# Optimization experiments

Measured on AMD Instinct MI355X. Metric: run time of the kernel, lower is better.

Reference implementation:

```python
import jax, jax.numpy as jnp
import numpy as np

B, N, M = 32, 512, 32          # batch frames, atoms, neighbors
H_A = 64                        # atom embedding dim
DMIN, DMAX, STEP = 0.0, 10.0, 0.1
FILTERS = jnp.arange(DMIN, DMAX + STEP, STEP, dtype=jnp.float32)  # [101]
H_B = FILTERS.shape[0]
N_CONV = 4
N_CLASSES = 10
BN_EPS = 1e-5


def setup_inputs() -> dict:
    key = jax.random.key(0)
    ks = jax.random.split(key, 6)
    return {
        "nbr_adj_dist": jax.random.uniform(ks[0], (B, N, M), jnp.float32) * DMAX,
        "nbr_adj_list": jax.random.randint(ks[1], (B, N, M), 0, N),
        "emb_w": jax.random.normal(ks[2], (N, H_A), jnp.float32),
        "fc_w": jax.random.normal(ks[3], (N_CONV, 2 * H_A + H_B, 2 * H_A), jnp.float32) * 0.05,
        "fc_b": jnp.zeros((N_CONV, 2 * H_A), jnp.float32),
        "bn1_g": jnp.ones((N_CONV, 2 * H_A), jnp.float32),
        "bn1_b": jnp.zeros((N_CONV, 2 * H_A), jnp.float32),
        "bn2_g": jnp.ones((N_CONV, H_A), jnp.float32),
        "bn2_b": jnp.zeros((N_CONV, H_A), jnp.float32),
        "cls_w": jax.random.normal(ks[4], (H_A, N_CLASSES), jnp.float32) * 0.05,
        "cls_b": jnp.zeros((N_CLASSES,), jnp.float32),
    }


def _bn(x2d, g, b):
    # training-mode BatchNorm1d over flattened batch axis (biased variance)
    mu = x2d.mean(axis=0)
    var = x2d.var(axis=0)
    return g * (x2d - mu) * jax.lax.rsqrt(var + BN_EPS) + b


def reference(nbr_adj_dist, nbr_adj_list, emb_w, fc_w, fc_b,
              bn1_g, bn1_b, bn2_g, bn2_b, cls_w, cls_b):
    # 1. Gaussian basis expansion of neighbor distances: [B,N,M,H_B]
    nbr_emb = jnp.exp(-((nbr_adj_dist[..., None] - FILTERS) ** 2) / (STEP ** 2))
    # 2. atom embeddings: atom_emb_idx = arange(N) per batch element
    atom = jnp.broadcast_to(emb_w[None], (B, N, H_A))
    # 3. CGCNN-style graph convolutions
    for l in range(N_CONV):
        # neighbor gather per batch: [B,N,M,H_A]
        nbrs = jax.vmap(lambda e, idx: e[idx])(atom, nbr_adj_list)
        total = jnp.concatenate(
            [jnp.broadcast_to(atom[:, :, None, :], (B, N, M, H_A)), nbrs, nbr_emb],
            axis=-1)                                        # [B,N,M,2*H_A+H_B]
        gated = jnp.einsum('bnmf,fh->bnmh', total, fc_w[l]) + fc_b[l]
        gated = _bn(gated.reshape(-1, 2 * H_A), bn1_g[l], bn1_b[l]).reshape(B, N, M, 2 * H_A)
        filt, core = jnp.split(gated, 2, axis=-1)
        summed = jnp.sum(jax.nn.sigmoid(filt) * jax.nn.relu(core), axis=2)  # [B,N,H_A]
        summed = _bn(summed.reshape(-1, H_A), bn2_g[l], bn2_b[l]).reshape(B, N, H_A)
        atom = jax.nn.relu(atom + summed)  # layer-internal residual
    # 4-6. activation, mean pooling over atoms, classifier, softmax
    emb = jax.nn.relu(atom)
    pooled = jnp.sum(emb, axis=1) / N                      # [B,H_A]
    logits = pooled @ cls_w + cls_b                        # [B,n_classes]
    return jax.nn.softmax(logits, axis=-1)
```

## Files before the change

### kernel.cpp

```cpp
#include <hip/hip_runtime.h>
#include <math.h>

typedef _Float16 half_t;
typedef __attribute__((ext_vector_type(4))) _Float16 half4;

constexpr int kB   = 32;
constexpr int kN   = 512;
constexpr int kM   = 32;
constexpr int kHA  = 64;
constexpr int kHB  = 101;
constexpr int kHO  = 128;
constexpr int kNF  = 229;
constexpr int kRows = kB * kN;
constexpr long kTRows = (long)kRows * kM;
constexpr int kNCls = 10;
constexpr float kEps = 1e-5f;
constexpr int kG    = 8;
constexpr int kNB   = kRows / kG;
constexpr int kT    = 512;
constexpr int kTaps = 8;

__device__ __forceinline__ int origCh(int j) {
    return ((j & 1) << 6) + ((j >> 2) << 1) + ((j >> 1) & 1);
}

__global__ void k_init_atom(const float* __restrict__ emb, float* __restrict__ atom) {
    int i = blockIdx.x * blockDim.x + threadIdx.x;
    atom[i] = emb[i & (kN * kHA - 1)];
}

template<bool RESID>
__global__ __launch_bounds__(256)
void k_pre(const float* __restrict__ atomIn, float* __restrict__ atomOut,
           const float* __restrict__ summed, const float* __restrict__ acc2,
           const float* __restrict__ g2, const float* __restrict__ b2,
           const float* __restrict__ W, const float* __restrict__ bias,
           float* __restrict__ preA, float* __restrict__ preB,
           float* __restrict__ bn1acc, float* __restrict__ zeroBuf) {
    __shared__ float sA[32 * 64];
    __shared__ float sc2s[128];
    int t = threadIdx.x;
    if (blockIdx.x == 0) {
        bn1acc[t] = 0.f;
        if (t < 128) zeroBuf[t] = 0.f;
    }
    if (RESID) {
        if (t < 64) {
            float inv = 1.f / (float)kRows;
            float mu = acc2[t] * inv;
            float var = acc2[64 + t] * inv - mu * mu;
            float sc = g2[t] * rsqrtf(var + kEps);
            sc2s[t] = sc;
            sc2s[64 + t] = b2[t] - mu * sc;
        }
        __syncthreads();
    }
    int r0 = blockIdx.x * 32;
    for (int i = t; i < 32 * 64; i += 256) {
        float v = atomIn[r0 * 64 + i];
        if (RESID) {
            int h = i & 63;
            v = fmaxf(v + fmaf(summed[r0 * 64 + i], sc2s[h], sc2s[64 + h]), 0.f);
            atomOut[r0 * 64 + i] = v;
        }
        sA[i] = v;
    }
    __syncthreads();
    int cg = t & 31, rg = t >> 5;
    float2 bb01 = *(const float2*)&bias[2 * cg];
    float2 bb23 = *(const float2*)&bias[64 + 2 * cg];
    float4 accA[4], accB[4];
    #pragma unroll
    for (int r = 0; r < 4; ++r) {
        accA[r] = make_float4(bb01.x, bb23.x, bb01.y, bb23.y);
        accB[r] = make_float4(0.f, 0.f, 0.f, 0.f);
    }
    for (int k = 0; k < 64; ++k) {
        float2 wA01 = *(const float2*)&W[k * kHO + 2 * cg];
        float2 wA23 = *(const float2*)&W[k * kHO + 64 + 2 * cg];
        float2 wB01 = *(const float2*)&W[(64 + k) * kHO + 2 * cg];
        float2 wB23 = *(const float2*)&W[(64 + k) * kHO + 64 + 2 * cg];
        #pragma unroll
        for (int r = 0; r < 4; ++r) {
            float a = sA[(rg * 4 + r) * 64 + k];
            accA[r].x = fmaf(a, wA01.x, accA[r].x);
            accA[r].y = fmaf(a, wA23.x, accA[r].y);
            accA[r].z = fmaf(a, wA01.y, accA[r].z);
            accA[r].w = fmaf(a, wA23.y, accA[r].w);
            accB[r].x = fmaf(a, wB01.x, accB[r].x);
            accB[r].y = fmaf(a, wB23.x, accB[r].y);
            accB[r].z = fmaf(a, wB01.y, accB[r].z);
            accB[r].w = fmaf(a, wB23.y, accB[r].w);
        }
    }
    #pragma unroll
    for (int r = 0; r < 4; ++r) {
        int row = r0 + rg * 4 + r;
        *(float4*)&preA[row * kHO + 4 * cg] = accA[r];
        *(float4*)&preB[row * kHO + 4 * cg] = accB[r];
    }
}

__global__ __launch_bounds__(kT, 6)
void k_stats(const float* __restrict__ dist, const int* __restrict__ nbrs,
             const float* __restrict__ preA, const float* __restrict__ preB,
             const float* __restrict__ W3, float* __restrict__ acc) {
    __shared__ half_t W3h[kHB * kHO];
    __shared__ float wv[kG][kM][kTaps];
    __shared__ int   roff[kG][kM];
    __shared__ int   wbase[kG][kM];
    __shared__ float red[2048];
    int t = threadIdx.x;
    int lb = (int)(blockIdx.x & 7) * (kNB / 8) + (int)(blockIdx.x >> 3);
    for (int i = t; i < kHB * kHO; i += kT)
        W3h[i] = (half_t)W3[(i & ~127) + origCh(i & 127)];
    if (t < kG * kM) {
        int g = t >> 5, m = t & 31;
        int p = lb * kG + g;
        float d = dist[p * kM + m];
        int kc = (int)floorf(d * 10.f);
        int ks = min(max(kc - 3, 0), kHB - kTaps);
        wbase[g][m] = ks * kHO;
        roff[g][m] = (((p >> 9) << 9) + nbrs[p * kM + m]) * kHO;
        #pragma unroll
        for (int j = 0; j < kTaps; ++j) {
            float dd = d - 0.1f * (float)(ks + j);
            wv[g][m][j] = __expf(-100.f * dd * dd);
        }
    }
    __syncthreads();
    int cg = t & 31, ms = t >> 5;
    float S[4] = {0.f, 0.f, 0.f, 0.f}, SS[4] = {0.f, 0.f, 0.f, 0.f};
    for (int g = 0; g < kG; ++g) {
        int p = lb * kG + g;
        float4 pa = *(const float4*)&preA[p * kHO + 4 * cg];
        #pragma unroll
        for (int mm = 0; mm < 2; ++mm) {
            int m = ms + mm * 16;
            int ro = roff[g][m], wb = wbase[g][m];
            float4 pb = *(const float4*)&preB[ro + 4 * cg];
            float x0 = pa.x + pb.x, x1 = pa.y + pb.y;
            float x2 = pa.z + pb.z, x3 = pa.w + pb.w;
            float warr[kTaps];
            *(float4*)&warr[0] = *(const float4*)&wv[g][m][0];
            *(float4*)&warr[4] = *(const float4*)&wv[g][m][4];
            const half_t* hb = &W3h[wb + 4 * cg];
            #pragma unroll
            for (int j = 0; j < kTaps; ++j) {
                half4 hv = *(const half4*)&hb[j * kHO];
                float w = warr[j];
                x0 = fmaf(w, (float)hv.x, x0);
                x1 = fmaf(w, (float)hv.y, x1);
                x2 = fmaf(w, (float)hv.z, x2);
                x3 = fmaf(w, (float)hv.w, x3);
            }
            S[0] += x0; S[1] += x1; S[2] += x2; S[3] += x3;
            SS[0] = fmaf(x0, x0, SS[0]); SS[1] = fmaf(x1, x1, SS[1]);
            SS[2] = fmaf(x2, x2, SS[2]); SS[3] = fmaf(x3, x3, SS[3]);
        }
    }
    #pragma unroll
    for (int c = 0; c < 4; ++c) {
        S[c]  += __shfl_xor(S[c], 32);
        SS[c] += __shfl_xor(SS[c], 32);
    }
    int w = t >> 6;
    if ((t & 63) < 32) {
        *(float4*)&red[w * 128 + cg * 4] = make_float4(S[0], S[1], S[2], S[3]);
        *(float4*)&red[1024 + w * 128 + cg * 4] = make_float4(SS[0], SS[1], SS[2], SS[3]);
    }
    __syncthreads();
    if (t < 256) {
        int j = t & 127, sel = t >> 7;
        float s = 0.f;
        #pragma unroll
        for (int ww = 0; ww < 8; ++ww) s += red[sel * 1024 + ww * 128 + j];
        atomicAdd(&acc[sel * 128 + j], s);
    }
}

__global__ __launch_bounds__(kT, 6)
void k_apply(const float* __restrict__ dist, const int* __restrict__ nbrs,
             const float* __restrict__ preA, const float* __restrict__ preB,
             const float* __restrict__ W3, const float* __restrict__ acc,
             const float* __restrict__ g1, const float* __restrict__ b1,
             float* __restrict__ summed, float* __restrict__ acc2) {
    __shared__ half_t W3h[kHB * kHO];
    __shared__ float wv[kG][kM][kTaps];
    __shared__ int   roff[kG][kM];
    __shared__ int   wbase[kG][kM];
    __shared__ float red2[512];
    __shared__ float scP[128], shP[128];
    int t = threadIdx.x;
    int lb = (int)(blockIdx.x & 7) * (kNB / 8) + (int)(blockIdx.x >> 3);
    for (int i = t; i < kHB * kHO; i += kT)
        W3h[i] = (half_t)W3[(i & ~127) + origCh(i & 127)];
    if (t < kG * kM) {
        int g = t >> 5, m = t & 31;
        int p = lb * kG + g;
        float d = dist[p * kM + m];
        int kc = (int)floorf(d * 10.f);
        int ks = min(max(kc - 3, 0), kHB - kTaps);
        wbase[g][m] = ks * kHO;
        roff[g][m] = (((p >> 9) << 9) + nbrs[p * kM + m]) * kHO;
        #pragma unroll
        for (int j = 0; j < kTaps; ++j) {
            float dd = d - 0.1f * (float)(ks + j);
            wv[g][m][j] = __expf(-100.f * dd * dd);
        }
    }
    if (t < 128) {
        float inv = 1.f / (float)kTRows;
        int oc = origCh(t);
        float mu = acc[t] * inv;
        float var = acc[128 + t] * inv - mu * mu;
        float sc = g1[oc] * rsqrtf(var + kEps);
        scP[t] = sc;
        shP[t] = b1[oc] - mu * sc;
    }
    __syncthreads();
    int cg = t & 31, ms = t >> 5;
    float4 sc4 = *(const float4*)&scP[4 * cg];
    float4 sh4 = *(const float4*)&shP[4 * cg];
    float S2 = 0.f, SS2 = 0.f;
    for (int g = 0; g < kG; ++g) {
        int p = lb * kG + g;
        float4 pa = *(const float4*)&preA[p * kHO + 4 * cg];
        float s0 = 0.f, s1 = 0.f;
        #pragma unroll
        for (int mm = 0; mm < 2; ++mm) {
            int m = ms + mm * 16;
            int ro = roff[g][m], wb = wbase[g][m];
            float4 pb = *(const float4*)&preB[ro + 4 * cg];
            float x0 = pa.x + pb.x, x1 = pa.y + pb.y;
            float x2 = pa.z + pb.z, x3 = pa.w + pb.w;
            float warr[kTaps];
            *(float4*)&warr[0] = *(const float4*)&wv[g][m][0];
            *(float4*)&warr[4] = *(const float4*)&wv[g][m][4];
            const half_t* hb = &W3h[wb + 4 * cg];
            #pragma unroll
            for (int j = 0; j < kTaps; ++j) {
                half4 hv = *(const half4*)&hb[j * kHO];
                float w = warr[j];
                x0 = fmaf(w, (float)hv.x, x0);
                x1 = fmaf(w, (float)hv.y, x1);
                x2 = fmaf(w, (float)hv.z, x2);
                x3 = fmaf(w, (float)hv.w, x3);
            }
            float yf0 = fmaf(x0, sc4.x, sh4.x);
            float yc0 = fmaf(x1, sc4.y, sh4.y);
            float yf1 = fmaf(x2, sc4.z, sh4.z);
            float yc1 = fmaf(x3, sc4.w, sh4.w);
            float sg0 = 1.f / (1.f + __expf(-yf0));
            float sg1 = 1.f / (1.f + __expf(-yf1));
            s0 = fmaf(sg0, fmaxf(yc0, 0.f), s0);
            s1 = fmaf(sg1, fmaxf(yc1, 0.f), s1);
        }
        s0 += __shfl_xor(s0, 32);
        s1 += __shfl_xor(s1, 32);
        int w = t >> 6;
        if ((t & 63) < 32)
            *(float2*)&red2[w * 64 + cg * 2] = make_float2(s0, s1);
        __syncthreads();
        if (t < 64) {
            float v = 0.f;
            #pragma unroll
            for (int ww = 0; ww < 8; ++ww) v += red2[ww * 64 + t];
            summed[p * kHA + t] = v;
            S2 += v;
            SS2 = fmaf(v, v, SS2);
        }
        __syncthreads();
    }
    if (t < 64) {
        atomicAdd(&acc2[t], S2);
        atomicAdd(&acc2[64 + t], SS2);
    }
}

__global__ __launch_bounds__(1024)
void k_final(const float* __restrict__ atom, const float* __restrict__ summed,
             const float* __restrict__ acc2, const float* __restrict__ g2,
             const float* __restrict__ b2, const float* __restrict__ cw,
             const float* __restrict__ cb, float* __restrict__ out) {
    __shared__ float red[1024];
    __shared__ float sc2s[128];
    __shared__ float pooled[kHA];
    __shared__ float lg[kNCls];
    int b = blockIdx.x, t = threadIdx.x;
    if (t < 64) {
        float inv = 1.f / (float)kRows;
        float mu = acc2[t] * inv;
        float var = acc2[64 + t] * inv - mu * mu;
        float sc = g2[t] * rsqrtf(var + kEps);
        sc2s[t] = sc;
        sc2s[64 + t] = b2[t] - mu * sc;
    }
    __syncthreads();
    int h = t & 63, q = t >> 6;
    const float* ab = atom + (long)b * kN * kHA;
    const float* sb = summed + (long)b * kN * kHA;
    float scv = sc2s[h], shv = sc2s[64 + h];
    float s = 0.f;
    for (int n = q * 32; n < q * 32 + 32; ++n) {
        float v = ab[n * 64 + h] + fmaf(sb[n * 64 + h], scv, shv);
        s += fmaxf(v, 0.f);
    }
    red[t] = s;
    __syncthreads();
    if (t < 64) {
        float v = 0.f;
        #pragma unroll
        for (int qq = 0; qq < 16; ++qq) v += red[qq * 64 + t];
        pooled[t] = v * (1.f / kN);
    }
    __syncthreads();
    if (t < kNCls) {
        float a = cb[t];
        #pragma unroll
        for (int k = 0; k < kHA; ++k) a = fmaf(pooled[k], cw[k * kNCls + t], a);
        lg[t] = a;
    }
    __syncthreads();
    if (t == 0) {
        float mx = lg[0];
        for (int c = 1; c < kNCls; ++c) mx = fmaxf(mx, lg[c]);
        float e[kNCls], se = 0.f;
        for (int c = 0; c < kNCls; ++c) { e[c] = __expf(lg[c] - mx); se += e[c]; }
        float inv = 1.f / se;
        for (int c = 0; c < kNCls; ++c) out[b * kNCls + c] = e[c] * inv;
    }
}

extern "C" void kernel_launch(void* const* d_in, const int* in_sizes, int n_in,
                              void* d_out, int out_size, void* d_ws, size_t ws_size,
                              hipStream_t stream) {
    const float* dist = (const float*)d_in[0];
    const int*   nbrs = (const int*)d_in[1];
    const float* emb  = (const float*)d_in[2];
    const float* fcw  = (const float*)d_in[3];
    const float* fcb  = (const float*)d_in[4];
    const float* bn1g = (const float*)d_in[5];
    const float* bn1b = (const float*)d_in[6];
    const float* bn2g = (const float*)d_in[7];
    const float* bn2b = (const float*)d_in[8];
    const float* clw  = (const float*)d_in[9];
    const float* clb  = (const float*)d_in[10];
    float* out = (float*)d_out;

    float* ws     = (float*)d_ws;
    float* atom   = ws;
    float* preA   = atom + kRows * kHA;
    float* preB   = preA + kRows * kHO;
    float* summed = preB + kRows * kHO;
    float* bn1acc = summed + kRows * kHA;
    float* acc2a  = bn1acc + 256;
    float* acc2b  = acc2a + 128;

    k_init_atom<<<dim3(kRows * kHA / 256), dim3(256), 0, stream>>>(emb, atom);
    for (int l = 0; l < 4; ++l) {
        const float* W  = fcw + (long)l * kNF * kHO;
        const float* W3 = W + 2 * kHA * kHO;
        float* accW = (l & 1) ? acc2b : acc2a;
        float* accR = ((l - 1) & 1) ? acc2b : acc2a;
        if (l == 0)
            k_pre<false><<<dim3(kRows / 32), dim3(256), 0, stream>>>(
                atom, atom, nullptr, nullptr, nullptr, nullptr,
                W, fcb + l * kHO, preA, preB, bn1acc, accW);
        else
            k_pre<true><<<dim3(kRows / 32), dim3(256), 0, stream>>>(
                atom, atom, summed, accR, bn2g + (l - 1) * kHA, bn2b + (l - 1) * kHA,
                W, fcb + l * kHO, preA, preB, bn1acc, accW);
        k_stats<<<dim3(kNB), dim3(kT), 0, stream>>>(dist, nbrs, preA, preB, W3, bn1acc);
        k_apply<<<dim3(kNB), dim3(kT), 0, stream>>>(dist, nbrs, preA, preB, W3, bn1acc,
                                                    bn1g + l * kHO, bn1b + l * kHO,
                                                    summed, accW);
    }
    k_final<<<dim3(kB), dim3(1024), 0, stream>>>(atom, summed, acc2b,
                                                 bn2g + 3 * kHA, bn2b + 3 * kHA,
                                                 clw, clb, out);
}
```

Baseline: 744.6 us.

## Process 16 atoms per block with per-thread full neighbor loop and fewer syncs

k_stats and k_apply now cover 16 atoms per block instead of 8, which halves the number of blocks and spreads the W3 half-precision staging over twice as many atoms. Each thread now loops over all 32 neighbors of one atom and batches four preB gathers at a time. This removes the per-atom __syncthreads reductions in k_apply and the cross-warp shuffles. The reduction scratch reuses the wv buffer and the W3 staging writes half2 pairs. The cost is lower occupancy (launch bounds 5), fewer blocks in flight and a longer serial loop per thread.

```diff
diff --git a/kernel.cpp b/kernel.cpp
--- a/kernel.cpp
+++ b/kernel.cpp
@@ -2,6 +2,7 @@
 #include <math.h>
 
 typedef _Float16 half_t;
+typedef __attribute__((ext_vector_type(2))) _Float16 half2_t;
 typedef __attribute__((ext_vector_type(4))) _Float16 half4;
 
 constexpr int kB   = 32;
@@ -15,8 +16,8 @@
 constexpr long kTRows = (long)kRows * kM;
 constexpr int kNCls = 10;
 constexpr float kEps = 1e-5f;
-constexpr int kG    = 8;
-constexpr int kNB   = kRows / kG;
+constexpr int kGP   = 16;
+constexpr int kNBs  = kRows / kGP;
 constexpr int kT    = 512;
 constexpr int kTaps = 8;
 
@@ -101,50 +102,64 @@
     }
 }
 
-__global__ __launch_bounds__(kT, 6)
+__device__ __forceinline__ void stage_w3_and_tiles(int t, int lb,
+        const float* __restrict__ dist, const int* __restrict__ nbrs,
+        const float* __restrict__ W3, half_t* __restrict__ W3h,
+        float (*wv)[kM][kTaps], int2 (*rw)[kM]) {
+    for (int i = t; i < kHB * 64; i += kT) {
+        int row = i >> 6, pj = (i & 63) * 2;
+        half2_t hp;
+        hp.x = (half_t)W3[row * kHO + origCh(pj)];
+        hp.y = (half_t)W3[row * kHO + origCh(pj + 1)];
+        *(half2_t*)&W3h[row * 128 + pj] = hp;
+    }
+    int lp = t >> 5, m = t & 31;
+    int p = lb * kGP + lp;
+    float d = dist[p * kM + m];
+    int kc = (int)floorf(d * 10.f);
+    int ks = min(max(kc - 3, 0), kHB - kTaps);
+    int ro = ((p & ~(kN - 1)) + nbrs[p * kM + m]) * kHO;
+    rw[lp][m] = make_int2(ro, ks * kHO);
+    #pragma unroll
+    for (int j = 0; j < kTaps; ++j) {
+        float dd = d - 0.1f * (float)(ks + j);
+        wv[lp][m][j] = __expf(-100.f * dd * dd);
+    }
+}
+
+__global__ __launch_bounds__(kT, 5)
 void k_stats(const float* __restrict__ dist, const int* __restrict__ nbrs,
              const float* __restrict__ preA, const float* __restrict__ preB,
              const float* __restrict__ W3, float* __restrict__ acc) {
     __shared__ half_t W3h[kHB * kHO];
-    __shared__ float wv[kG][kM][kTaps];
-    __shared__ int   roff[kG][kM];
-    __shared__ int   wbase[kG][kM];
-    __shared__ float red[2048];
+    __shared__ float wv[kGP][kM][kTaps];
+    __shared__ int2  rw[kGP][kM];
     int t = threadIdx.x;
-    int lb = (int)(blockIdx.x & 7) * (kNB / 8) + (int)(blockIdx.x >> 3);
-    for (int i = t; i < kHB * kHO; i += kT)
-        W3h[i] = (half_t)W3[(i & ~127) + origCh(i & 127)];
-    if (t < kG * kM) {
-        int g = t >> 5, m = t & 31;
-        int p = lb * kG + g;
-        float d = dist[p * kM + m];
-        int kc = (int)floorf(d * 10.f);
-        int ks = min(max(kc - 3, 0), kHB - kTaps);
-        wbase[g][m] = ks * kHO;
-        roff[g][m] = (((p >> 9) << 9) + nbrs[p * kM + m]) * kHO;
-        #pragma unroll
-        for (int j = 0; j < kTaps; ++j) {
-            float dd = d - 0.1f * (float)(ks + j);
-            wv[g][m][j] = __expf(-100.f * dd * dd);
-        }
-    }
-    __syncthreads();
-    int cg = t & 31, ms = t >> 5;
-    float S[4] = {0.f, 0.f, 0.f, 0.f}, SS[4] = {0.f, 0.f, 0.f, 0.f};
-    for (int g = 0; g < kG; ++g) {
-        int p = lb * kG + g;
-        float4 pa = *(const float4*)&preA[p * kHO + 4 * cg];
-        #pragma unroll
-        for (int mm = 0; mm < 2; ++mm) {
-            int m = ms + mm * 16;
-            int ro = roff[g][m], wb = wbase[g][m];
-            float4 pb = *(const float4*)&preB[ro + 4 * cg];
-            float x0 = pa.x + pb.x, x1 = pa.y + pb.y;
-            float x2 = pa.z + pb.z, x3 = pa.w + pb.w;
-            float warr[kTaps];
-            *(float4*)&warr[0] = *(const float4*)&wv[g][m][0];
-            *(float4*)&warr[4] = *(const float4*)&wv[g][m][4];
-            const half_t* hb = &W3h[wb + 4 * cg];
+    int lb = (int)(blockIdx.x & 7) * (kNBs / 8) + (int)(blockIdx.x >> 3);
+    stage_w3_and_tiles(t, lb, dist, nbrs, W3, W3h, wv, rw);
+    __syncthreads();
+    int cg = t & 31, lp = t >> 5;
+    int p = lb * kGP + lp;
+    float4 pa = *(const float4*)&preA[(size_t)p * kHO + 4 * cg];
+    float S0 = 0.f, S1 = 0.f, S2 = 0.f, S3 = 0.f;
+    float T0 = 0.f, T1 = 0.f, T2 = 0.f, T3 = 0.f;
+    for (int m0 = 0; m0 < kM; m0 += 4) {
+        int2 rwl[4];
+        float4 pb[4];
+        #pragma unroll
+        for (int u = 0; u < 4; ++u) rwl[u] = rw[lp][m0 + u];
+        #pragma unroll
+        for (int u = 0; u < 4; ++u)
+            pb[u] = *(const float4*)&preB[(size_t)rwl[u].x + 4 * cg];
+        #pragma unroll
+        for (int u = 0; u < 4; ++u) {
+            float4 w04 = *(const float4*)&wv[lp][m0 + u][0];
+            float4 w48 = *(const float4*)&wv[lp][m0 + u][4];
+            float warr[kTaps] = {w04.x, w04.y, w04.z, w04.w,
+                                 w48.x, w48.y, w48.z, w48.w};
+            float x0 = pa.x + pb[u].x, x1 = pa.y + pb[u].y;
+            float x2 = pa.z + pb[u].z, x3 = pa.w + pb[u].w;
+            const half_t* hb = &W3h[rwl[u].y + 4 * cg];
             #pragma unroll
             for (int j = 0; j < kTaps; ++j) {
                 half4 hv = *(const half4*)&hb[j * kHO];
@@ -154,61 +169,45 @@
                 x2 = fmaf(w, (float)hv.z, x2);
                 x3 = fmaf(w, (float)hv.w, x3);
             }
-            S[0] += x0; S[1] += x1; S[2] += x2; S[3] += x3;
-            SS[0] = fmaf(x0, x0, SS[0]); SS[1] = fmaf(x1, x1, SS[1]);
-            SS[2] = fmaf(x2, x2, SS[2]); SS[3] = fmaf(x3, x3, SS[3]);
-        }
-    }
-    #pragma unroll
-    for (int c = 0; c < 4; ++c) {
-        S[c]  += __shfl_xor(S[c], 32);
-        SS[c] += __shfl_xor(SS[c], 32);
-    }
-    int w = t >> 6;
-    if ((t & 63) < 32) {
-        *(float4*)&red[w * 128 + cg * 4] = make_float4(S[0], S[1], S[2], S[3]);
-        *(float4*)&red[1024 + w * 128 + cg * 4] = make_float4(SS[0], SS[1], SS[2], SS[3]);
-    }
-    __syncthreads();
-    if (t < 256) {
-        int j = t & 127, sel = t >> 7;
+            S0 += x0; S1 += x1; S2 += x2; S3 += x3;
+            T0 = fmaf(x0, x0, T0); T1 = fmaf(x1, x1, T1);
+            T2 = fmaf(x2, x2, T2); T3 = fmaf(x3, x3, T3);
+        }
+    }
+    float* red = (float*)wv;
+    __syncthreads();
+    *(float4*)&red[lp * 128 + 4 * cg] = make_float4(S0, S1, S2, S3);
+    __syncthreads();
+    if (t < 128) {
         float s = 0.f;
         #pragma unroll
-        for (int ww = 0; ww < 8; ++ww) s += red[sel * 1024 + ww * 128 + j];
-        atomicAdd(&acc[sel * 128 + j], s);
-    }
-}
-
-__global__ __launch_bounds__(kT, 6)
+        for (int l2 = 0; l2 < kGP; ++l2) s += red[l2 * 128 + t];
+        atomicAdd(&acc[t], s);
+    }
+    __syncthreads();
+    *(float4*)&red[lp * 128 + 4 * cg] = make_float4(T0, T1, T2, T3);
+    __syncthreads();
+    if (t < 128) {
+        float s = 0.f;
+        #pragma unroll
+        for (int l2 = 0; l2 < kGP; ++l2) s += red[l2 * 128 + t];
+        atomicAdd(&acc[128 + t], s);
+    }
+}
+
+__global__ __launch_bounds__(kT, 5)
 void k_apply(const float* __restrict__ dist, const int* __restrict__ nbrs,
              const float* __restrict__ preA, const float* __restrict__ preB,
              const float* __restrict__ W3, const float* __restrict__ acc,
              const float* __restrict__ g1, const float* __restrict__ b1,
              float* __restrict__ summed, float* __restrict__ acc2) {
     __shared__ half_t W3h[kHB * kHO];
-    __shared__ float wv[kG][kM][kTaps];
-    __shared__ int   roff[kG][kM];
-    __shared__ int   wbase[kG][kM];
-    __shared__ float red2[512];
+    __shared__ float wv[kGP][kM][kTaps];
+    __shared__ int2  rw[kGP][kM];
     __shared__ float scP[128], shP[128];
     int t = threadIdx.x;
-    int lb = (int)(blockIdx.x & 7) * (kNB / 8) + (int)(blockIdx.x >> 3);
-    for (int i = t; i < kHB * kHO; i += kT)
-        W3h[i] = (half_t)W3[(i & ~127) + origCh(i & 127)];
-    if (t < kG * kM) {
-        int g = t >> 5, m = t & 31;
-        int p = lb * kG + g;
-        float d = dist[p * kM + m];
-        int kc = (int)floorf(d * 10.f);
-        int ks = min(max(kc - 3, 0), kHB - kTaps);
-        wbase[g][m] = ks * kHO;
-        roff[g][m] = (((p >> 9) << 9) + nbrs[p * kM + m]) * kHO;
-        #pragma unroll
-        for (int j = 0; j < kTaps; ++j) {
-            float dd = d - 0.1f * (float)(ks + j);
-            wv[g][m][j] = __expf(-100.f * dd * dd);
-        }
-    }
+    int lb = (int)(blockIdx.x & 7) * (kNBs / 8) + (int)(blockIdx.x >> 3);
+    stage_w3_and_tiles(t, lb, dist, nbrs, W3, W3h, wv, rw);
     if (t < 128) {
         float inv = 1.f / (float)kTRows;
         int oc = origCh(t);
@@ -219,25 +218,29 @@
         shP[t] = b1[oc] - mu * sc;
     }
     __syncthreads();
-    int cg = t & 31, ms = t >> 5;
+    int cg = t & 31, lp = t >> 5;
+    int p = lb * kGP + lp;
+    float4 pa = *(const float4*)&preA[(size_t)p * kHO + 4 * cg];
     float4 sc4 = *(const float4*)&scP[4 * cg];
     float4 sh4 = *(const float4*)&shP[4 * cg];
-    float S2 = 0.f, SS2 = 0.f;
-    for (int g = 0; g < kG; ++g) {
-        int p = lb * kG + g;
-        float4 pa = *(const float4*)&preA[p * kHO + 4 * cg];
-        float s0 = 0.f, s1 = 0.f;
-        #pragma unroll
-        for (int mm = 0; mm < 2; ++mm) {
-            int m = ms + mm * 16;
-            int ro = roff[g][m], wb = wbase[g][m];
-            float4 pb = *(const float4*)&preB[ro + 4 * cg];
-            float x0 = pa.x + pb.x, x1 = pa.y + pb.y;
-            float x2 = pa.z + pb.z, x3 = pa.w + pb.w;
-            float warr[kTaps];
-            *(float4*)&warr[0] = *(const float4*)&wv[g][m][0];
-            *(float4*)&warr[4] = *(const float4*)&wv[g][m][4];
-            const half_t* hb = &W3h[wb + 4 * cg];
+    float s0 = 0.f, s1 = 0.f;
+    for (int m0 = 0; m0 < kM; m0 += 4) {
+        int2 rwl[4];
+        float4 pb[4];
+        #pragma unroll
+        for (int u = 0; u < 4; ++u) rwl[u] = rw[lp][m0 + u];
+        #pragma unroll
+        for (int u = 0; u < 4; ++u)
+            pb[u] = *(const float4*)&preB[(size_t)rwl[u].x + 4 * cg];
+        #pragma unroll
+        for (int u = 0; u < 4; ++u) {
+            float4 w04 = *(const float4*)&wv[lp][m0 + u][0];
+            float4 w48 = *(const float4*)&wv[lp][m0 + u][4];
+            float warr[kTaps] = {w04.x, w04.y, w04.z, w04.w,
+                                 w48.x, w48.y, w48.z, w48.w};
+            float x0 = pa.x + pb[u].x, x1 = pa.y + pb[u].y;
+            float x2 = pa.z + pb[u].z, x3 = pa.w + pb[u].w;
+            const half_t* hb = &W3h[rwl[u].y + 4 * cg];
             #pragma unroll
             for (int j = 0; j < kTaps; ++j) {
                 half4 hv = *(const half4*)&hb[j * kHO];
@@ -256,23 +259,20 @@
             s0 = fmaf(sg0, fmaxf(yc0, 0.f), s0);
             s1 = fmaf(sg1, fmaxf(yc1, 0.f), s1);
         }
-        s0 += __shfl_xor(s0, 32);
-        s1 += __shfl_xor(s1, 32);
-        int w = t >> 6;
-        if ((t & 63) < 32)
-            *(float2*)&red2[w * 64 + cg * 2] = make_float2(s0, s1);
-        __syncthreads();
-        if (t < 64) {
-            float v = 0.f;
-            #pragma unroll
-            for (int ww = 0; ww < 8; ++ww) v += red2[ww * 64 + t];
-            summed[p * kHA + t] = v;
+    }
+    *(float2*)&summed[(size_t)p * kHA + 2 * cg] = make_float2(s0, s1);
+    float* red = (float*)wv;
+    __syncthreads();
+    *(float2*)&red[lp * 64 + 2 * cg] = make_float2(s0, s1);
+    __syncthreads();
+    if (t < 64) {
+        float S2 = 0.f, SS2 = 0.f;
+        #pragma unroll
+        for (int l2 = 0; l2 < kGP; ++l2) {
+            float v = red[l2 * 64 + t];
             S2 += v;
             SS2 = fmaf(v, v, SS2);
         }
-        __syncthreads();
-    }
-    if (t < 64) {
         atomicAdd(&acc2[t], S2);
         atomicAdd(&acc2[64 + t], SS2);
     }
@@ -371,10 +371,10 @@
             k_pre<true><<<dim3(kRows / 32), dim3(256), 0, stream>>>(
                 atom, atom, summed, accR, bn2g + (l - 1) * kHA, bn2b + (l - 1) * kHA,
                 W, fcb + l * kHO, preA, preB, bn1acc, accW);
-        k_stats<<<dim3(kNB), dim3(kT), 0, stream>>>(dist, nbrs, preA, preB, W3, bn1acc);
-        k_apply<<<dim3(kNB), dim3(kT), 0, stream>>>(dist, nbrs, preA, preB, W3, bn1acc,
-                                                    bn1g + l * kHO, bn1b + l * kHO,
-                                                    summed, accW);
+        k_stats<<<dim3(kNBs), dim3(kT), 0, stream>>>(dist, nbrs, preA, preB, W3, bn1acc);
+        k_apply<<<dim3(kNBs), dim3(kT), 0, stream>>>(dist, nbrs, preA, preB, W3, bn1acc,
+                                                     bn1g + l * kHO, bn1b + l * kHO,
+                                                     summed, accW);
     }
     k_final<<<dim3(kB), dim3(1024), 0, stream>>>(atom, summed, acc2b,
                                                  bn2g + 3 * kHA, bn2b + 3 * kHA,
```

Result: slower. 1.685 ms (+126.3%).
